# Optimization experiments

Hardware: AMD Instinct MI355X
Metric: run time of the kernel (lower is better)

The kernel has to match this reference:

```python
import jax, jax.numpy as jnp
import numpy as np

BATCH, SEQ, DIM, DSTATE = 8, 2048, 1024, 16


def setup_inputs() -> dict:
    key = jax.random.key(0)
    ks = jax.random.split(key, 8)
    u = jax.random.normal(ks[0], (BATCH, SEQ, DIM), jnp.float32)
    gate = jax.random.normal(ks[1], (BATCH, SEQ, DIM), jnp.float32)
    # parameters (init per module: normal std=0.01 for A_log/B/C, zeros for D)
    A_log = 0.01 * jax.random.normal(ks[2], (DSTATE, DSTATE), jnp.float32)
    B_mat = 0.01 * jax.random.normal(ks[3], (DIM, DSTATE), jnp.float32)
    C_mat = 0.01 * jax.random.normal(ks[4], (DIM, DSTATE), jnp.float32)
    D = jnp.zeros((DIM,), jnp.float32)
    bound = 1.0 / np.sqrt(DIM)  # nn.Linear default init
    dt_w = jax.random.uniform(ks[5], (1, DIM), jnp.float32, -bound, bound)
    dt_b = jax.random.uniform(ks[6], (1,), jnp.float32, -bound, bound)
    return {"u": u, "gate": gate, "A_log": A_log, "B_mat": B_mat,
            "C_mat": C_mat, "D": D, "dt_w": dt_w, "dt_b": dt_b}


def reference(u, gate, A_log, B_mat, C_mat, D, dt_w, dt_b):
    # delta = sigmoid(Linear(gate)) : [B, S, 1] -> [B, S]
    delta = jax.nn.sigmoid(jnp.einsum('bsd,od->bso', gate, dt_w) + dt_b)[..., 0]
    A = -jnp.exp(A_log)                               # [N, N]
    scaled_A = delta[..., None, None] * A             # [B, S, N, N]
    A_exp = jax.scipy.linalg.expm(scaled_A)           # batched matrix exp
    Bu = jnp.einsum('bsd,dn->bsn', u, B_mat)          # [B, S, N]

    def step(h, inp):
        Aexp_t, bu_t = inp                            # [B,N,N], [B,N]
        h = jnp.einsum('bn,bnm->bm', h, Aexp_t) + bu_t
        return h, h

    h0 = jnp.zeros((u.shape[0], DSTATE), u.dtype)
    _, hs = jax.lax.scan(step, h0, (jnp.swapaxes(A_exp, 0, 1), jnp.swapaxes(Bu, 0, 1)))
    hs = jnp.swapaxes(hs, 0, 1)                       # [B, S, N]
    y = jnp.einsum('bsn,dn->bsd', hs, C_mat) + D * u  # [B, S, D]
    return y
```

## Files before the change

### kernel.cpp

```cpp
#include <hip/hip_runtime.h>

#define BATCH  8
#define SEQ    2048
#define DIMSZ  1024
#define NST    16
#define LCH    32
#define CPB    (SEQ / LCH)
#define NCHUNK (BATCH * CPB)
#define NCHEB  32
#define PI_F   3.14159265358979f

typedef __attribute__((ext_vector_type(8))) short bf16x8;
typedef __attribute__((ext_vector_type(4))) float f32x4;

static __device__ __forceinline__ unsigned short f2bf(float f) {
    unsigned u = __builtin_bit_cast(unsigned, f);
    unsigned r = (u + 0x7FFFu + ((u >> 16) & 1u)) >> 16;
    return (unsigned short)r;
}
static __device__ __forceinline__ float bf2f(unsigned short h) {
    unsigned u = ((unsigned)h) << 16;
    return __builtin_bit_cast(float, u);
}

__global__ __launch_bounds__(256) void k1_setup_delta(
    const float* __restrict__ gate, const float* __restrict__ dt_w,
    const float* __restrict__ dt_b, const float* __restrict__ A_log,
    const float* __restrict__ B_mat,
    float* __restrict__ delta, float* __restrict__ Gt,
    unsigned short* __restrict__ Bfh, unsigned short* __restrict__ Bfl)
{
    __shared__ float Fn_l[32 * 256];
    __shared__ float XT[4][2][272];
    __shared__ float cosT[32 * 32];
    const int tid  = threadIdx.x;
    const int lane = tid & 63;
    const int w    = tid >> 6;
    const int g    = blockIdx.x;

    if (g > 0) {
        const int tok  = (g - 1) * 4 + w;
        const float* gp = gate + (size_t)tok * DIMSZ;
        float s = 0.f;
#pragma unroll
        for (int i = 0; i < 4; ++i) {
            const float4 gv = *(const float4*)(gp   + i * 256 + lane * 4);
            const float4 wv = *(const float4*)(dt_w + i * 256 + lane * 4);
            s = fmaf(gv.x, wv.x, s); s = fmaf(gv.y, wv.y, s);
            s = fmaf(gv.z, wv.z, s); s = fmaf(gv.w, wv.w, s);
        }
#pragma unroll
        for (int off = 32; off >= 1; off >>= 1)
            s += __shfl_xor(s, off, 64);
        if (lane == 0)
            delta[tok] = 1.0f / (1.0f + expf(-(s + dt_b[0])));
        return;
    }

    float* Xw = &XT[w][0][0];
    float* Tw = &XT[w][1][0];
    const int jb = lane & 15;
    const int ib = lane >> 4;
    for (int nn = 0; nn < 8; ++nn) {
        const int node = w * 8 + nn;
        const float th = (2.f * node + 1.f) * (PI_F / 64.f);
        const float dn = 0.5f * (1.f + cosf(th));
        float S[4];
#pragma unroll
        for (int p = 0; p < 4; ++p) {
            const int e = lane + 64 * p;
            const int i = ib + 4 * p;
            const float a = -expf(A_log[e]);
            const float x = dn * a * (1.0f / 64.0f);
            Xw[i * 17 + jb] = x;
            Tw[i * 17 + jb] = x;
            S[p] = x + (i == jb ? 1.0f : 0.0f);
        }
        __syncthreads();
#pragma unroll
        for (int k = 2; k <= 8; ++k) {
            float nt[4];
#pragma unroll
            for (int p = 0; p < 4; ++p) {
                const int i = ib + 4 * p;
                float acc = 0.f;
#pragma unroll
                for (int kk = 0; kk < 16; ++kk)
                    acc = fmaf(Tw[i * 17 + kk], Xw[kk * 17 + jb], acc);
                nt[p] = acc * (1.0f / (float)k);
                S[p] += nt[p];
            }
            __syncthreads();
#pragma unroll
            for (int p = 0; p < 4; ++p)
                Tw[(ib + 4 * p) * 17 + jb] = nt[p];
            __syncthreads();
        }
#pragma unroll
        for (int r = 0; r < 6; ++r) {
            __syncthreads();
#pragma unroll
            for (int p = 0; p < 4; ++p)
                Tw[(ib + 4 * p) * 17 + jb] = S[p];
            __syncthreads();
#pragma unroll
            for (int p = 0; p < 4; ++p) {
                const int i = ib + 4 * p;
                float acc = 0.f;
#pragma unroll
                for (int kk = 0; kk < 16; ++kk)
                    acc = fmaf(Tw[i * 17 + kk], Tw[kk * 17 + jb], acc);
                S[p] = acc;
            }
        }
#pragma unroll
        for (int p = 0; p < 4; ++p)
            Fn_l[node * 256 + lane + 64 * p] = S[p];
    }
#pragma unroll
    for (int p = 0; p < 4; ++p) {
        const int idx = tid * 4 + p;
        const int m = idx >> 5, k = idx & 31;
        const float th = (2.f * k + 1.f) * (PI_F / 64.f);
        cosT[idx] = cosf((float)m * th);
    }
    __syncthreads();
    {
        float acc[NCHEB];
#pragma unroll
        for (int m = 0; m < NCHEB; ++m) acc[m] = 0.f;
        for (int k = 0; k < NCHEB; ++k) {
            const float f = Fn_l[k * 256 + tid];
#pragma unroll
            for (int m = 0; m < NCHEB; ++m)
                acc[m] = fmaf(f, cosT[m * 32 + k], acc[m]);
        }
#pragma unroll
        for (int m = 0; m < NCHEB; ++m) {
            const float sc = (m == 0) ? (1.f / 32.f) : (2.f / 32.f);
            Gt[(size_t)tid * NCHEB + m] = acc[m] * sc;
        }
    }
    for (int t = 0; t < 64; ++t) {
        const int idx = t * 256 + tid;
        const int j  = idx & 7;
        const int l  = (idx >> 3) & 63;
        const int ks = idx >> 9;
        const int k  = ks * 32 + ((l >> 4) << 3) + j;
        const int n  = l & 15;
        float bv = B_mat[(size_t)k * 16 + n];
        unsigned short h = f2bf(bv);
        Bfh[idx] = h;
        Bfl[idx] = f2bf(bv - bf2f(h));
    }
}

__global__ __launch_bounds__(256, 2) void kBA(
    const float* __restrict__ u,
    const unsigned short* __restrict__ Bfh, const unsigned short* __restrict__ Bfl,
    const float* __restrict__ Gt, const float* __restrict__ delta,
    float* __restrict__ Bu, float* __restrict__ P, float* __restrict__ e)
{
    __shared__ float smem[8704];
    __shared__ float Bus[LCH * NST];
    __shared__ float dl[LCH];
    __shared__ float sd[1];
    __shared__ float Ps[16 * 17];
    const int tid  = threadIdx.x;
    const int lane = tid & 63;
    const int w    = tid >> 6;
    const size_t gI = blockIdx.x;
    const int tok0 = (int)gI * 32;
    const int half = w & 1;
    const int wrow = (w >> 1) * 16;
    const int q    = lane >> 4;
    const int r    = lane & 15;

    if (tid < LCH) dl[tid] = delta[gI * LCH + tid];

    const uint4* bh = (const uint4*)Bfh;
    const uint4* bl = (const uint4*)Bfl;

    const int srow = 8 * w + (lane >> 5);
    const int p    = lane & 31;
    int colb[4];
#pragma unroll
    for (int i = 0; i < 4; ++i) {
        const int row = srow + 2 * i;
        const int lc  = (p & 16) | ((p & 15) ^ (row & 15));
        colb[i] = ((lc & 16) ? 512 : 0) + (lc & 15) * 4;
    }

    auto stage = [&](int c, int b) {
#pragma unroll
        for (int i = 0; i < 4; ++i) {
            const float* gp = u + (size_t)(tok0 + srow + 2 * i) * DIMSZ
                                + (colb[i] + c * 64);
            __builtin_amdgcn_global_load_lds(
                (const __attribute__((address_space(1))) void*)gp,
                (__attribute__((address_space(3))) void*)&smem[b * 4096 + (8 * w + 2 * i) * 128],
                16, 0, 0);
        }
    };

    f32x4 acc = {0.f, 0.f, 0.f, 0.f};
    uint4 fh[2][2], fl[2][2];

    stage(0, 0);
    stage(1, 1);
    {
        const int ks0 = half * 16;
        fh[0][0] = bh[(ks0 + 0) * 64 + lane]; fl[0][0] = bl[(ks0 + 0) * 64 + lane];
        fh[0][1] = bh[(ks0 + 1) * 64 + lane]; fl[0][1] = bl[(ks0 + 1) * 64 + lane];
    }
    asm volatile("s_waitcnt vmcnt(8)" ::: "memory");
    __builtin_amdgcn_sched_barrier(0);
    __builtin_amdgcn_s_barrier();

#pragma unroll
    for (int c = 0; c < 8; ++c) {
        const int b = c & 1;
        float fu[2][8];
#pragma unroll
        for (int s = 0; s < 2; ++s) {
            const int c16a = (s * 8 + 2 * q + 0) ^ r;
            const int c16b = (s * 8 + 2 * q + 1) ^ r;
            const float4 v0 = *(const float4*)&smem[b * 4096 + (wrow + r) * 128 + (half * 16 + c16a) * 4];
            const float4 v1 = *(const float4*)&smem[b * 4096 + (wrow + r) * 128 + (half * 16 + c16b) * 4];
            fu[s][0] = v0.x; fu[s][1] = v0.y; fu[s][2] = v0.z; fu[s][3] = v0.w;
            fu[s][4] = v1.x; fu[s][5] = v1.y; fu[s][6] = v1.z; fu[s][7] = v1.w;
        }
        asm volatile("s_waitcnt lgkmcnt(0)" ::: "memory");
        __builtin_amdgcn_sched_barrier(0);
        __builtin_amdgcn_s_barrier();
        if (c + 2 < 8) stage(c + 2, b);
        if (c + 1 < 8) {
            const int ks0 = half * 16 + 2 * (c + 1);
            fh[(c + 1) & 1][0] = bh[(ks0 + 0) * 64 + lane];
            fl[(c + 1) & 1][0] = bl[(ks0 + 0) * 64 + lane];
            fh[(c + 1) & 1][1] = bh[(ks0 + 1) * 64 + lane];
            fl[(c + 1) & 1][1] = bl[(ks0 + 1) * 64 + lane];
        }
        __builtin_amdgcn_sched_barrier(0);
#pragma unroll
        for (int s = 0; s < 2; ++s) {
            bf16x8 uh, ul;
#pragma unroll
            for (int i = 0; i < 8; ++i) {
                unsigned short h = f2bf(fu[s][i]);
                uh[i] = (short)h;
                ul[i] = (short)f2bf(fu[s][i] - bf2f(h));
            }
            const bf16x8 Bh = __builtin_bit_cast(bf16x8, fh[b][s]);
            const bf16x8 Bl = __builtin_bit_cast(bf16x8, fl[b][s]);
            acc = __builtin_amdgcn_mfma_f32_16x16x32_bf16(uh, Bh, acc, 0, 0, 0);
            acc = __builtin_amdgcn_mfma_f32_16x16x32_bf16(uh, Bl, acc, 0, 0, 0);
            acc = __builtin_amdgcn_mfma_f32_16x16x32_bf16(ul, Bh, acc, 0, 0, 0);
        }
        if (c < 7) {
            if (c < 6) asm volatile("s_waitcnt vmcnt(8)" ::: "memory");
            else       asm volatile("s_waitcnt vmcnt(4)" ::: "memory");
            __builtin_amdgcn_sched_barrier(0);
            __builtin_amdgcn_s_barrier();
        }
    }

    float* red = smem;
#pragma unroll
    for (int rr = 0; rr < 4; ++rr)
        red[w * 256 + (q * 4 + rr) * 16 + r] = acc[rr];
    __syncthreads();
    const float b0 = red[tid]       + red[256 + tid];
    const float b1 = red[512 + tid] + red[768 + tid];
    Bu[gI * 512 + tid]       = b0;
    Bu[gI * 512 + 256 + tid] = b1;
    Bus[tid]       = b0;
    Bus[256 + tid] = b1;

    float gr[NCHEB];
    {
        const float4* gp = (const float4*)(Gt + (size_t)tid * NCHEB);
#pragma unroll
        for (int qq = 0; qq < NCHEB / 4; ++qq) {
            float4 v = gp[qq];
            gr[qq*4+0] = v.x; gr[qq*4+1] = v.y; gr[qq*4+2] = v.z; gr[qq*4+3] = v.w;
        }
    }
    __syncthreads();
    if (tid == 0) {
        float s = 0.f;
        for (int t = 0; t < LCH; ++t) s += dl[t];
        sd[0] = s;
    }
    for (int t = 0; t < LCH; ++t) {
        const float x = 2.f * dl[t] - 1.f;
        float accm = fmaf(gr[1], x, gr[0]);
        float tm2 = 1.f, tm1 = x;
#pragma unroll
        for (int m = 2; m < NCHEB; ++m) {
            const float tm = fmaf(2.f * x, tm1, -tm2);
            accm = fmaf(gr[m], tm, accm);
            tm2 = tm1; tm1 = tm;
        }
        smem[t * 272 + (tid >> 4) * 17 + (tid & 15)] = accm;
    }
    __syncthreads();
    float S;
    {
        const float xp = 2.f * (sd[0] * (1.f / LCH)) - 1.f;
        float accm = fmaf(gr[1], xp, gr[0]);
        float tm2 = 1.f, tm1 = xp;
#pragma unroll
        for (int m = 2; m < NCHEB; ++m) {
            const float tm = fmaf(2.f * xp, tm1, -tm2);
            accm = fmaf(gr[m], tm, accm);
            tm2 = tm1; tm1 = tm;
        }
        S = accm;
    }
    const int i = tid >> 4, j = tid & 15;
#pragma unroll
    for (int rr = 0; rr < 5; ++rr) {
        Ps[i*17 + j] = S;
        __syncthreads();
        float ns = 0.f;
#pragma unroll
        for (int k = 0; k < 16; ++k)
            ns = fmaf(Ps[i*17 + k], Ps[k*17 + j], ns);
        __syncthreads();
        S = ns;
    }
    P[gI * 256 + tid] = S;
    if (tid < 64) {
        const int gq = tid >> 4, jj = tid & 15, i0 = gq * 4;
        float h = 0.f;
        for (int t = 0; t < LCH; ++t) {
            float pp = 0.f;
#pragma unroll
            for (int m = 0; m < 4; ++m)
                pp = fmaf(__shfl(h, gq * 20 + m, 64),
                          smem[t * 272 + (i0 + m) * 17 + jj], pp);
            pp += __shfl_xor(pp, 16, 64);
            pp += __shfl_xor(pp, 32, 64);
            h = Bus[t * 16 + jj] + pp;
        }
        if (gq == 0) e[gI * NST + jj] = h;
    }
}

__global__ __launch_bounds__(256) void k4_scan(
    const float* __restrict__ P, const float* __restrict__ e,
    float* __restrict__ hin)
{
    __shared__ float Pl[32 * 272];
    __shared__ float el[32 * NST];
    const int tid = threadIdx.x;
    const int b = blockIdx.x;
    float h = 0.f;
    for (int half = 0; half < 2; ++half) {
        const int c0 = half * 32;
        for (int idx = tid; idx < 32*256; idx += 256) {
            const int c = idx >> 8, ij = idx & 255, i = ij >> 4, jj = ij & 15;
            Pl[c*272 + i*17 + jj] = P[((size_t)(b*CPB + c0 + c)) * 256 + ij];
        }
        for (int idx = tid; idx < 32*NST; idx += 256)
            el[idx] = e[((size_t)(b*CPB + c0)) * NST + idx];
        __syncthreads();
        if (tid < 64) {
            const int gq = tid >> 4, j = tid & 15, i0 = gq * 4;
            for (int c = 0; c < 32; ++c) {
                if (tid < 16) hin[((size_t)(b*CPB + c0 + c)) * NST + j] = h;
                float pp = 0.f;
#pragma unroll
                for (int m = 0; m < 4; ++m)
                    pp = fmaf(__shfl(h, gq * 20 + m, 64),
                              Pl[c*272 + (i0 + m)*17 + j], pp);
                pp += __shfl_xor(pp, 16, 64);
                pp += __shfl_xor(pp, 32, 64);
                h = el[c*16 + j] + pp;
            }
        }
        __syncthreads();
    }
}

__global__ __launch_bounds__(256) void k5_out(
    const float* __restrict__ Gt, const float* __restrict__ delta,
    const float* __restrict__ Bu, const float* __restrict__ hin,
    const float* __restrict__ u, const float* __restrict__ C_mat,
    const float* __restrict__ D, float* __restrict__ y)
{
    __shared__ float Mlds[32 * 272];
    __shared__ float Bus[LCH * NST];
    __shared__ float dl[LCH];
    __shared__ __align__(16) float Hs[LCH * NST];
    const int tid = threadIdx.x;
    const size_t g = blockIdx.x;
    if (tid < LCH) dl[tid] = delta[g * LCH + tid];
    for (int idx = tid; idx < LCH * NST; idx += 256)
        Bus[idx] = Bu[g * (size_t)(LCH * NST) + idx];
    float gr[NCHEB];
    {
        const float4* gp = (const float4*)(Gt + (size_t)tid * NCHEB);
#pragma unroll
        for (int qq = 0; qq < NCHEB / 4; ++qq) {
            float4 v = gp[qq];
            gr[qq*4+0] = v.x; gr[qq*4+1] = v.y; gr[qq*4+2] = v.z; gr[qq*4+3] = v.w;
        }
    }
    __syncthreads();
    for (int t = 0; t < LCH; ++t) {
        const float x = 2.f * dl[t] - 1.f;
        float accm = fmaf(gr[1], x, gr[0]);
        float tm2 = 1.f, tm1 = x;
#pragma unroll
        for (int m = 2; m < NCHEB; ++m) {
            const float tm = fmaf(2.f * x, tm1, -tm2);
            accm = fmaf(gr[m], tm, accm);
            tm2 = tm1; tm1 = tm;
        }
        Mlds[t * 272 + (tid >> 4) * 17 + (tid & 15)] = accm;
    }
    __syncthreads();
    if (tid < 64) {
        const int gq = tid >> 4, jj = tid & 15, i0 = gq * 4;
        float h = hin[g * NST + jj];
        for (int t = 0; t < LCH; ++t) {
            float pp = 0.f;
#pragma unroll
            for (int m = 0; m < 4; ++m)
                pp = fmaf(__shfl(h, gq * 20 + m, 64),
                          Mlds[t * 272 + (i0 + m) * 17 + jj], pp);
            pp += __shfl_xor(pp, 16, 64);
            pp += __shfl_xor(pp, 32, 64);
            h = Bus[t * 16 + jj] + pp;
            if (gq == 0) Hs[t * 16 + jj] = h;
        }
    }
    __syncthreads();
    const int d0 = tid * 4;
    float4 cr[4][4];
#pragma unroll
    for (int r = 0; r < 4; ++r)
#pragma unroll
        for (int qq = 0; qq < 4; ++qq)
            cr[r][qq] = ((const float4*)C_mat)[(d0 + r) * 4 + qq];
    const float4 dv = ((const float4*)D)[tid];
    const bool dnz = (dv.x != 0.f) || (dv.y != 0.f) || (dv.z != 0.f) || (dv.w != 0.f);
    for (int t = 0; t < LCH; ++t) {
        const size_t row = (g * LCH + t) * DIMSZ;
        float y0 = 0.f, y1 = 0.f, y2 = 0.f, y3 = 0.f;
        if (dnz) {
            const float4 uv = ((const float4*)(u + row))[tid];
            y0 = dv.x * uv.x; y1 = dv.y * uv.y; y2 = dv.z * uv.z; y3 = dv.w * uv.w;
        }
#pragma unroll
        for (int qq = 0; qq < 4; ++qq) {
            const float4 hq = *((const float4*)&Hs[t*16 + qq*4]);
            y0 = fmaf(hq.x, cr[0][qq].x, y0); y0 = fmaf(hq.y, cr[0][qq].y, y0);
            y0 = fmaf(hq.z, cr[0][qq].z, y0); y0 = fmaf(hq.w, cr[0][qq].w, y0);
            y1 = fmaf(hq.x, cr[1][qq].x, y1); y1 = fmaf(hq.y, cr[1][qq].y, y1);
            y1 = fmaf(hq.z, cr[1][qq].z, y1); y1 = fmaf(hq.w, cr[1][qq].w, y1);
            y2 = fmaf(hq.x, cr[2][qq].x, y2); y2 = fmaf(hq.y, cr[2][qq].y, y2);
            y2 = fmaf(hq.z, cr[2][qq].z, y2); y2 = fmaf(hq.w, cr[2][qq].w, y2);
            y3 = fmaf(hq.x, cr[3][qq].x, y3); y3 = fmaf(hq.y, cr[3][qq].y, y3);
            y3 = fmaf(hq.w, cr[3][qq].w, y3); y3 = fmaf(hq.z, cr[3][qq].z, y3);
        }
        float4 ov; ov.x = y0; ov.y = y1; ov.z = y2; ov.w = y3;
        ((float4*)(y + row))[tid] = ov;
    }
}

extern "C" void kernel_launch(void* const* d_in, const int* in_sizes, int n_in,
                              void* d_out, int out_size, void* d_ws, size_t ws_size,
                              hipStream_t stream)
{
    const float* u     = (const float*)d_in[0];
    const float* gate  = (const float*)d_in[1];
    const float* A_log = (const float*)d_in[2];
    const float* B_mat = (const float*)d_in[3];
    const float* C_mat = (const float*)d_in[4];
    const float* D     = (const float*)d_in[5];
    const float* dt_w  = (const float*)d_in[6];
    const float* dt_b  = (const float*)d_in[7];
    float* y = (float*)d_out;

    float* ws = (float*)d_ws;
    size_t o = 0;
    float* Gt    = ws + o; o += 256 * NCHEB;
    float* delta = ws + o; o += (size_t)BATCH * SEQ;
    float* Bu    = ws + o; o += (size_t)BATCH * SEQ * NST;
    float* P     = ws + o; o += (size_t)NCHUNK * 256;
    float* e     = ws + o; o += (size_t)NCHUNK * NST;
    float* hin   = ws + o; o += (size_t)NCHUNK * NST;
    unsigned short* Bfh = (unsigned short*)(ws + o); o += 8192;
    unsigned short* Bfl = (unsigned short*)(ws + o); o += 8192;

    k1_setup_delta<<<BATCH * SEQ / 4 + 1, 256, 0, stream>>>(
        gate, dt_w, dt_b, A_log, B_mat, delta, Gt, Bfh, Bfl);
    kBA    <<<NCHUNK, 256, 0, stream>>>(u, Bfh, Bfl, Gt, delta, Bu, P, e);
    k4_scan<<<BATCH,  256, 0, stream>>>(P, e, hin);
    k5_out <<<NCHUNK, 256, 0, stream>>>(Gt, delta, Bu, hin, u, C_mat, D, y);
}
```

Measured before the change: 286.1 us.

## Fuse delta computation into chunk kernel and widen single-block setup to 512 threads

Moves the per-token gate·dt_w dot product and sigmoid out of the setup kernel's 4096 extra blocks and into the chunk kernel, where each block computes delta for its own 32 tokens before staging u. The setup kernel now runs as one 512-thread block, halving the serial per-wave matrix-power and Chebyshev work by spreading nodes and output coefficients over 8 waves. The goal is to shorten the serial single-block critical path and remove one pass over delta, at the cost of adding gate reads and a barrier at the start of the chunk kernel. A reordering of two FMAs in the output kernel restores consistent accumulation order.

```diff
diff --git a/kernel.cpp b/kernel.cpp
--- a/kernel.cpp
+++ b/kernel.cpp
@@ -23,46 +23,23 @@
     return __builtin_bit_cast(float, u);
 }
 
-__global__ __launch_bounds__(256) void k1_setup_delta(
-    const float* __restrict__ gate, const float* __restrict__ dt_w,
-    const float* __restrict__ dt_b, const float* __restrict__ A_log,
-    const float* __restrict__ B_mat,
-    float* __restrict__ delta, float* __restrict__ Gt,
+__global__ __launch_bounds__(512) void kSetup(
+    const float* __restrict__ A_log, const float* __restrict__ B_mat,
+    float* __restrict__ Gt,
     unsigned short* __restrict__ Bfh, unsigned short* __restrict__ Bfl)
 {
     __shared__ float Fn_l[32 * 256];
-    __shared__ float XT[4][2][272];
+    __shared__ float XT[8][2][272];
     __shared__ float cosT[32 * 32];
     const int tid  = threadIdx.x;
     const int lane = tid & 63;
     const int w    = tid >> 6;
-    const int g    = blockIdx.x;
-
-    if (g > 0) {
-        const int tok  = (g - 1) * 4 + w;
-        const float* gp = gate + (size_t)tok * DIMSZ;
-        float s = 0.f;
-#pragma unroll
-        for (int i = 0; i < 4; ++i) {
-            const float4 gv = *(const float4*)(gp   + i * 256 + lane * 4);
-            const float4 wv = *(const float4*)(dt_w + i * 256 + lane * 4);
-            s = fmaf(gv.x, wv.x, s); s = fmaf(gv.y, wv.y, s);
-            s = fmaf(gv.z, wv.z, s); s = fmaf(gv.w, wv.w, s);
-        }
-#pragma unroll
-        for (int off = 32; off >= 1; off >>= 1)
-            s += __shfl_xor(s, off, 64);
-        if (lane == 0)
-            delta[tok] = 1.0f / (1.0f + expf(-(s + dt_b[0])));
-        return;
-    }
-
     float* Xw = &XT[w][0][0];
     float* Tw = &XT[w][1][0];
     const int jb = lane & 15;
     const int ib = lane >> 4;
-    for (int nn = 0; nn < 8; ++nn) {
-        const int node = w * 8 + nn;
+    for (int nn = 0; nn < 4; ++nn) {
+        const int node = w * 4 + nn;
         const float th = (2.f * node + 1.f) * (PI_F / 64.f);
         const float dn = 0.5f * (1.f + cosf(th));
         float S[4];
@@ -118,31 +95,34 @@
             Fn_l[node * 256 + lane + 64 * p] = S[p];
     }
 #pragma unroll
-    for (int p = 0; p < 4; ++p) {
-        const int idx = tid * 4 + p;
+    for (int t = 0; t < 2; ++t) {
+        const int idx = t * 512 + tid;
         const int m = idx >> 5, k = idx & 31;
         const float th = (2.f * k + 1.f) * (PI_F / 64.f);
         cosT[idx] = cosf((float)m * th);
     }
     __syncthreads();
     {
-        float acc[NCHEB];
-#pragma unroll
-        for (int m = 0; m < NCHEB; ++m) acc[m] = 0.f;
+        const int elem = tid & 255;
+        const int mg   = tid >> 8;
+        float acc[16];
+#pragma unroll
+        for (int mm = 0; mm < 16; ++mm) acc[mm] = 0.f;
         for (int k = 0; k < NCHEB; ++k) {
-            const float f = Fn_l[k * 256 + tid];
-#pragma unroll
-            for (int m = 0; m < NCHEB; ++m)
-                acc[m] = fmaf(f, cosT[m * 32 + k], acc[m]);
-        }
-#pragma unroll
-        for (int m = 0; m < NCHEB; ++m) {
+            const float f = Fn_l[k * 256 + elem];
+#pragma unroll
+            for (int mm = 0; mm < 16; ++mm)
+                acc[mm] = fmaf(f, cosT[(mg * 16 + mm) * 32 + k], acc[mm]);
+        }
+#pragma unroll
+        for (int mm = 0; mm < 16; ++mm) {
+            const int m = mg * 16 + mm;
             const float sc = (m == 0) ? (1.f / 32.f) : (2.f / 32.f);
-            Gt[(size_t)tid * NCHEB + m] = acc[m] * sc;
-        }
-    }
-    for (int t = 0; t < 64; ++t) {
-        const int idx = t * 256 + tid;
+            Gt[(size_t)elem * NCHEB + m] = acc[mm] * sc;
+        }
+    }
+    for (int t = 0; t < 32; ++t) {
+        const int idx = t * 512 + tid;
         const int j  = idx & 7;
         const int l  = (idx >> 3) & 63;
         const int ks = idx >> 9;
@@ -155,11 +135,13 @@
     }
 }
 
-__global__ __launch_bounds__(256, 2) void kBA(
-    const float* __restrict__ u,
+__global__ __launch_bounds__(256, 2) void kBD(
+    const float* __restrict__ u, const float* __restrict__ gate,
+    const float* __restrict__ dt_w, const float* __restrict__ dt_b,
     const unsigned short* __restrict__ Bfh, const unsigned short* __restrict__ Bfl,
-    const float* __restrict__ Gt, const float* __restrict__ delta,
-    float* __restrict__ Bu, float* __restrict__ P, float* __restrict__ e)
+    const float* __restrict__ Gt,
+    float* __restrict__ delta, float* __restrict__ Bu,
+    float* __restrict__ P, float* __restrict__ e)
 {
     __shared__ float smem[8704];
     __shared__ float Bus[LCH * NST];
@@ -176,7 +158,35 @@
     const int q    = lane >> 4;
     const int r    = lane & 15;
 
-    if (tid < LCH) dl[tid] = delta[gI * LCH + tid];
+    {
+        float4 wv[4];
+#pragma unroll
+        for (int i = 0; i < 4; ++i)
+            wv[i] = *(const float4*)(dt_w + i * 256 + lane * 4);
+        const float bias = dt_b[0];
+#pragma unroll
+        for (int tt = 0; tt < 8; ++tt) {
+            const int trow = w * 8 + tt;
+            const float* gp2 = gate + (size_t)(tok0 + trow) * DIMSZ;
+            float s = 0.f;
+#pragma unroll
+            for (int i = 0; i < 4; ++i) {
+                const float4 gv = *(const float4*)(gp2 + i * 256 + lane * 4);
+                s = fmaf(gv.x, wv[i].x, s); s = fmaf(gv.y, wv[i].y, s);
+                s = fmaf(gv.z, wv[i].z, s); s = fmaf(gv.w, wv[i].w, s);
+            }
+#pragma unroll
+            for (int off = 32; off >= 1; off >>= 1)
+                s += __shfl_xor(s, off, 64);
+            if (lane == 0) {
+                const float dv = 1.0f / (1.0f + expf(-(s + bias)));
+                dl[trow] = dv;
+                delta[gI * LCH + trow] = dv;
+            }
+        }
+    }
+    asm volatile("s_waitcnt vmcnt(0)" ::: "memory");
+    __syncthreads();
 
     const uint4* bh = (const uint4*)Bfh;
     const uint4* bl = (const uint4*)Bfl;
@@ -464,7 +474,7 @@
             y2 = fmaf(hq.x, cr[2][qq].x, y2); y2 = fmaf(hq.y, cr[2][qq].y, y2);
             y2 = fmaf(hq.z, cr[2][qq].z, y2); y2 = fmaf(hq.w, cr[2][qq].w, y2);
             y3 = fmaf(hq.x, cr[3][qq].x, y3); y3 = fmaf(hq.y, cr[3][qq].y, y3);
-            y3 = fmaf(hq.w, cr[3][qq].w, y3); y3 = fmaf(hq.z, cr[3][qq].z, y3);
+            y3 = fmaf(hq.z, cr[3][qq].z, y3); y3 = fmaf(hq.w, cr[3][qq].w, y3);
         }
         float4 ov; ov.x = y0; ov.y = y1; ov.z = y2; ov.w = y3;
         ((float4*)(y + row))[tid] = ov;
@@ -496,9 +506,9 @@
     unsigned short* Bfh = (unsigned short*)(ws + o); o += 8192;
     unsigned short* Bfl = (unsigned short*)(ws + o); o += 8192;
 
-    k1_setup_delta<<<BATCH * SEQ / 4 + 1, 256, 0, stream>>>(
-        gate, dt_w, dt_b, A_log, B_mat, delta, Gt, Bfh, Bfl);
-    kBA    <<<NCHUNK, 256, 0, stream>>>(u, Bfh, Bfl, Gt, delta, Bu, P, e);
+    kSetup <<<1,      512, 0, stream>>>(A_log, B_mat, Gt, Bfh, Bfl);
+    kBD    <<<NCHUNK, 256, 0, stream>>>(u, gate, dt_w, dt_b, Bfh, Bfl, Gt,
+                                        delta, Bu, P, e);
     k4_scan<<<BATCH,  256, 0, stream>>>(P, e, hin);
     k5_out <<<NCHUNK, 256, 0, stream>>>(Gt, delta, Bu, hin, u, C_mat, D, y);
 }
```

Result: no change. 285.1 us (-0.3%).
